# Kernel optimization log

Measured on AMD Instinct MI355X. Metric: run time of the kernel, lower is better.

The kernel has to match this reference:

```python
import jax, jax.numpy as jnp
import numpy as np

N, IN_F, OUT_F = 8192, 256, 128
ALPHA = 0.2          # LeakyReLU negative slope
NEG_INF = -9e15      # mask value used by the original module
DENSITY = 0.1        # adjacency density


def setup_inputs() -> dict:
    key = jax.random.key(0)
    k1, k2, k3, k4 = jax.random.split(key, 4)
    x = jax.random.normal(k1, (N, IN_F), dtype=jnp.float32)
    adj = (jax.random.uniform(k2, (N, N)) < DENSITY).astype(jnp.float32)
    W = jax.random.normal(k3, (IN_F, OUT_F), dtype=jnp.float32) * (1.0 / np.sqrt(IN_F))
    a = jax.random.normal(k4, (2 * OUT_F, 1), dtype=jnp.float32) * (1.0 / np.sqrt(2 * OUT_F))
    return {"x": x, "adj": adj, "W": W, "a": a}


def reference(x, adj, W, a):
    # h = x @ W : [N, F]
    h = x @ W
    # Decompose a^T [h_i ; h_j] = (h a1)_i + (h a2)_j  -- identical math to the
    # original O(N^2 * 2F) cat/repeat construction, without materializing it.
    a1 = a[:OUT_F, 0]           # [F]
    a2 = a[OUT_F:, 0]           # [F]
    s1 = h @ a1                 # [N]
    s2 = h @ a2                 # [N]
    e = jax.nn.leaky_relu(s1[:, None] + s2[None, :], negative_slope=ALPHA)  # [N, N]
    scores = jnp.where(adj > 0, e, NEG_INF)
    attention = jax.nn.softmax(scores, axis=1)   # row-wise softmax
    # dropout = 0.0 (eval mode) -> identity
    h_prime = attention @ h      # [N, F]
    return h_prime
```

## Files before the change

### kernel.cpp

```cpp
#include <hip/hip_runtime.h>
#include <hip/hip_bf16.h>

typedef __attribute__((ext_vector_type(4))) float  f32x4;
typedef __attribute__((ext_vector_type(8))) short  bf16x8;
typedef unsigned short u16;

#define ALPHA 0.2f
#define NN 8192
#define FF 128

extern "C" __global__ void __launch_bounds__(256)
gat_pre(const float* __restrict__ x, const float* __restrict__ Wm,
        const float* __restrict__ av, u16* __restrict__ hT,
        float* __restrict__ s1v, float* __restrict__ s2v) {
  __shared__ float xs[16][256];
  __shared__ float hs[16][128];
  const int t  = threadIdx.x;
  const int i0 = blockIdx.x * 16;

  {
    const int r = t >> 4, c0 = (t & 15) * 16;
    const f32x4* src = (const f32x4*)(x + (size_t)(i0 + r) * 256 + c0);
    f32x4* dst = (f32x4*)&xs[r][c0];
#pragma unroll
    for (int m = 0; m < 4; ++m) dst[m] = src[m];
  }
  __syncthreads();

  {
    const int c = t & 127, rh = t >> 7;
    float acc[8] = {0.f,0.f,0.f,0.f,0.f,0.f,0.f,0.f};
    for (int k = 0; k < 256; ++k) {
      const float wk = Wm[k * 128 + c];
#pragma unroll
      for (int r = 0; r < 8; ++r) acc[r] = fmaf(xs[rh * 8 + r][k], wk, acc[r]);
    }
#pragma unroll
    for (int r = 0; r < 8; ++r) hs[rh * 8 + r][c] = acc[r];
  }
  __syncthreads();

  {
    const int c = t >> 1, rr = (t & 1) * 8;
    u16 u[8];
#pragma unroll
    for (int k = 0; k < 8; ++k) {
      __hip_bfloat16 b = __float2bfloat16(hs[rr + k][c]);
      u[k] = *reinterpret_cast<u16*>(&b);
    }
    *(uint4*)(hT + (size_t)c * NN + i0 + rr) = *(const uint4*)u;
  }

  {
    const int r = t >> 4, q = t & 15;
    float p1 = 0.f, p2 = 0.f;
#pragma unroll
    for (int m = 0; m < 8; ++m) {
      const int c = q * 8 + m;
      const float hv = hs[r][c];
      p1 = fmaf(hv, av[c], p1);
      p2 = fmaf(hv, av[128 + c], p2);
    }
    p1 += __shfl_xor(p1, 1); p1 += __shfl_xor(p1, 2);
    p1 += __shfl_xor(p1, 4); p1 += __shfl_xor(p1, 8);
    p2 += __shfl_xor(p2, 1); p2 += __shfl_xor(p2, 2);
    p2 += __shfl_xor(p2, 4); p2 += __shfl_xor(p2, 8);
    if (q == 0) { s1v[i0 + r] = p1; s2v[i0 + r] = p2; }
  }
}

extern "C" __global__ void __launch_bounds__(512)
gat_main(const float* __restrict__ adj, const u16* __restrict__ hT,
         const float* __restrict__ s1v, const float* __restrict__ s2v,
         float* __restrict__ out) {
  __shared__ u16  wlds[32 * 128];
  __shared__ u16  hlds[128 * 128];
  __shared__ float denl[32];

  const int t    = threadIdx.x;
  const int lane = t & 63;
  const int i0   = blockIdx.x * 32;
  const int li   = t >> 4;
  const int j8   = (t & 15) * 8;
  const int wid  = t >> 6;
  const int rs   = wid & 1;
  const int cq   = wid >> 1;
  const int hc   = t >> 2;
  const int hq   = t & 3;

  const float s1i = s1v[i0 + li];
  const float* adjrow = adj + (size_t)(i0 + li) * NN + j8;
  const u16*   hrow   = hT + (size_t)hc * NN + hq * 32;

  f32x4 acc0 = {0.f,0.f,0.f,0.f}, acc1 = {0.f,0.f,0.f,0.f};
  float den = 0.f;

  f32x4 a0 = *(const f32x4*)(adjrow);
  f32x4 a1 = *(const f32x4*)(adjrow + 4);
  f32x4 z0 = *(const f32x4*)(s2v + j8);
  f32x4 z1 = *(const f32x4*)(s2v + j8 + 4);
  uint4 hr0 = *(const uint4*)(hrow);
  uint4 hr1 = *(const uint4*)(hrow + 8);
  uint4 hr2 = *(const uint4*)(hrow + 16);
  uint4 hr3 = *(const uint4*)(hrow + 24);

  for (int js = 0; js < NN; js += 128) {
    __syncthreads();

    {
      bf16x8 wpack;
      float dstep = 0.f;
#pragma unroll
      for (int e = 0; e < 8; ++e) {
        const float adv = (e < 4) ? a0[e] : a1[e - 4];
        const float tz  = s1i + ((e < 4) ? z0[e] : z1[e - 4]);
        const float fz  = tz > 0.f ? tz : ALPHA * tz;
        const float w8  = adv > 0.f ? __expf(fz) : 0.f;
        dstep += w8;
        __hip_bfloat16 hb = __float2bfloat16(w8);
        wpack[e] = *reinterpret_cast<short*>(&hb);
      }
      den += dstep;
      *(bf16x8*)((char*)wlds + ((li * 256 + j8 * 2) ^ ((li & 7) << 4))) = wpack;

      char* hb = (char*)hlds;
      const int base = hc * 256 + hq * 64;
      const int sw   = (hc & 7) << 4;
      *(uint4*)(hb + ((base +  0) ^ sw)) = hr0;
      *(uint4*)(hb + ((base + 16) ^ sw)) = hr1;
      *(uint4*)(hb + ((base + 32) ^ sw)) = hr2;
      *(uint4*)(hb + ((base + 48) ^ sw)) = hr3;
    }
    __syncthreads();

    if (js + 128 < NN) {
      const float* ap = adjrow + js + 128;
      a0 = *(const f32x4*)(ap);
      a1 = *(const f32x4*)(ap + 4);
      const float* zp = s2v + js + 128 + j8;
      z0 = *(const f32x4*)(zp);
      z1 = *(const f32x4*)(zp + 4);
      const u16* hp2 = hrow + js + 128;
      hr0 = *(const uint4*)(hp2);
      hr1 = *(const uint4*)(hp2 + 8);
      hr2 = *(const uint4*)(hp2 + 16);
      hr3 = *(const uint4*)(hp2 + 24);
    }

#pragma unroll
    for (int ks = 0; ks < 4; ++ks) {
      const int arow = rs * 16 + (lane & 15);
      const int koff = (ks * 32 + ((lane >> 4) << 3)) * 2;
      const bf16x8 af = *(const bf16x8*)((char*)wlds +
                          ((arow * 256 + koff) ^ ((arow & 7) << 4)));
      const int bc0 = cq * 32 + (lane & 15);
      const bf16x8 b0 = *(const bf16x8*)((char*)hlds +
                          ((bc0 * 256 + koff) ^ ((bc0 & 7) << 4)));
      const int bc1 = bc0 + 16;
      const bf16x8 b1 = *(const bf16x8*)((char*)hlds +
                          ((bc1 * 256 + koff) ^ ((bc1 & 7) << 4)));
      acc0 = __builtin_amdgcn_mfma_f32_16x16x32_bf16(af, b0, acc0, 0, 0, 0);
      acc1 = __builtin_amdgcn_mfma_f32_16x16x32_bf16(af, b1, acc1, 0, 0, 0);
    }
  }

  den += __shfl_xor(den, 1); den += __shfl_xor(den, 2);
  den += __shfl_xor(den, 4); den += __shfl_xor(den, 8);
  if ((t & 15) == 0) denl[li] = den;
  __syncthreads();

#pragma unroll
  for (int r = 0; r < 4; ++r) {
    const int row  = rs * 16 + ((lane >> 4) << 2) + r;
    const float dv = denl[row];
    const int col0 = cq * 32 + (lane & 15);
    out[(size_t)(i0 + row) * FF + col0]      = acc0[r] / dv;
    out[(size_t)(i0 + row) * FF + col0 + 16] = acc1[r] / dv;
  }
}

extern "C" void kernel_launch(void* const* d_in, const int* in_sizes, int n_in,
                              void* d_out, int out_size, void* d_ws, size_t ws_size,
                              hipStream_t stream) {
  const float* x   = (const float*)d_in[0];
  const float* adj = (const float*)d_in[1];
  const float* Wm  = (const float*)d_in[2];
  const float* av  = (const float*)d_in[3];
  float* out = (float*)d_out;

  u16*   hT  = (u16*)d_ws;
  float* s1v = (float*)((char*)d_ws + (size_t)FF * NN * 2);
  float* s2v = s1v + NN;

  gat_pre <<<NN / 16, 256, 0, stream>>>(x, Wm, av, hT, s1v, s2v);
  gat_main<<<NN / 32, 512, 0, stream>>>(adj, hT, s1v, s2v, out);
}
```

Measured before the change: 442.2 us.

## Split K across waves with direct global B-fragment loads and LDS reduction

Restructures the attention-aggregation kernel so that each of the 8 waves in a block handles a distinct slice of the neighbour (K) dimension for 16 rows. B fragments of hT are loaded straight from global memory into registers, which removes the per-iteration LDS staging and both __syncthreads. Partial accumulators and denominators are then reduced through LDS once at the end. The change also folds log2(e) into the precomputed scores so exp2 can be used, and replaces the adjacency branch with a multiply. The cost is more hT traffic through L2, since each block now rereads all of hT, and fewer rows per block.

```diff
diff --git a/kernel.cpp b/kernel.cpp
--- a/kernel.cpp
+++ b/kernel.cpp
@@ -8,6 +8,13 @@
 #define ALPHA 0.2f
 #define NN 8192
 #define FF 128
+#define LOG2E 1.4426950408889634f
+
+#if __has_builtin(__builtin_amdgcn_exp2f)
+#define EXP2F(x) __builtin_amdgcn_exp2f(x)
+#else
+#define EXP2F(x) __expf((x) * 0.6931471805599453f)
+#endif
 
 extern "C" __global__ void __launch_bounds__(256)
 gat_pre(const float* __restrict__ x, const float* __restrict__ Wm,
@@ -65,117 +72,97 @@
     p1 += __shfl_xor(p1, 4); p1 += __shfl_xor(p1, 8);
     p2 += __shfl_xor(p2, 1); p2 += __shfl_xor(p2, 2);
     p2 += __shfl_xor(p2, 4); p2 += __shfl_xor(p2, 8);
-    if (q == 0) { s1v[i0 + r] = p1; s2v[i0 + r] = p2; }
+    if (q == 0) { s1v[i0 + r] = p1 * LOG2E; s2v[i0 + r] = p2 * LOG2E; }
   }
 }
 
-extern "C" __global__ void __launch_bounds__(512)
+extern "C" __global__ void __launch_bounds__(512, 4)
 gat_main(const float* __restrict__ adj, const u16* __restrict__ hT,
-         const float* __restrict__ s1v, const float* __restrict__ s2v,
+         const float* __restrict__ s1l, const float* __restrict__ s2l,
          float* __restrict__ out) {
-  __shared__ u16  wlds[32 * 128];
-  __shared__ u16  hlds[128 * 128];
-  __shared__ float denl[32];
+  __shared__ float accp[8][16][132];
+  __shared__ float denp[8][16];
 
   const int t    = threadIdx.x;
   const int lane = t & 63;
-  const int i0   = blockIdx.x * 32;
-  const int li   = t >> 4;
-  const int j8   = (t & 15) * 8;
-  const int wid  = t >> 6;
-  const int rs   = wid & 1;
-  const int cq   = wid >> 1;
-  const int hc   = t >> 2;
-  const int hq   = t & 3;
+  const int wv   = t >> 6;
+  const int cA   = lane & 15;
+  const int kg   = lane >> 4;
+  const int i0   = blockIdx.x * 16;
+  const int jq0  = wv * (NN / 8);
 
-  const float s1i = s1v[i0 + li];
-  const float* adjrow = adj + (size_t)(i0 + li) * NN + j8;
-  const u16*   hrow   = hT + (size_t)hc * NN + hq * 32;
+  const float s1i = s1l[i0 + cA];
+  const float* adjp = adj + (size_t)(i0 + cA) * NN + jq0 + kg * 8;
+  const float* s2p  = s2l + jq0 + kg * 8;
+  const u16*   hTb  = hT + (size_t)cA * NN + jq0 + kg * 8;
 
-  f32x4 acc0 = {0.f,0.f,0.f,0.f}, acc1 = {0.f,0.f,0.f,0.f};
+  f32x4 acc[8];
+#pragma unroll
+  for (int f = 0; f < 8; ++f) acc[f] = (f32x4){0.f, 0.f, 0.f, 0.f};
   float den = 0.f;
 
-  f32x4 a0 = *(const f32x4*)(adjrow);
-  f32x4 a1 = *(const f32x4*)(adjrow + 4);
-  f32x4 z0 = *(const f32x4*)(s2v + j8);
-  f32x4 z1 = *(const f32x4*)(s2v + j8 + 4);
-  uint4 hr0 = *(const uint4*)(hrow);
-  uint4 hr1 = *(const uint4*)(hrow + 8);
-  uint4 hr2 = *(const uint4*)(hrow + 16);
-  uint4 hr3 = *(const uint4*)(hrow + 24);
+  f32x4 a0 = *(const f32x4*)(adjp);
+  f32x4 a1 = *(const f32x4*)(adjp + 4);
+  f32x4 z0 = *(const f32x4*)(s2p);
+  f32x4 z1 = *(const f32x4*)(s2p + 4);
 
-  for (int js = 0; js < NN; js += 128) {
-    __syncthreads();
+  for (int st = 0; st < 32; ++st) {
+    bf16x8 bf[8];
+#pragma unroll
+    for (int f = 0; f < 8; ++f)
+      bf[f] = *(const bf16x8*)(hTb + (size_t)f * 16 * NN + st * 32);
 
-    {
-      bf16x8 wpack;
-      float dstep = 0.f;
+    bf16x8 af;
+    float dstep = 0.f;
 #pragma unroll
-      for (int e = 0; e < 8; ++e) {
-        const float adv = (e < 4) ? a0[e] : a1[e - 4];
-        const float tz  = s1i + ((e < 4) ? z0[e] : z1[e - 4]);
-        const float fz  = tz > 0.f ? tz : ALPHA * tz;
-        const float w8  = adv > 0.f ? __expf(fz) : 0.f;
-        dstep += w8;
-        __hip_bfloat16 hb = __float2bfloat16(w8);
-        wpack[e] = *reinterpret_cast<short*>(&hb);
-      }
-      den += dstep;
-      *(bf16x8*)((char*)wlds + ((li * 256 + j8 * 2) ^ ((li & 7) << 4))) = wpack;
+    for (int e = 0; e < 8; ++e) {
+      const float adv = (e < 4) ? a0[e] : a1[e - 4];
+      const float tz  = s1i + ((e < 4) ? z0[e] : z1[e - 4]);
+      const float fz  = fmaxf(tz, ALPHA * tz);
+      const float w8  = adv * EXP2F(fz);
+      dstep += w8;
+      __hip_bfloat16 hb = __float2bfloat16(w8);
+      af[e] = *reinterpret_cast<short*>(&hb);
+    }
+    den += dstep;
 
-      char* hb = (char*)hlds;
-      const int base = hc * 256 + hq * 64;
-      const int sw   = (hc & 7) << 4;
-      *(uint4*)(hb + ((base +  0) ^ sw)) = hr0;
-      *(uint4*)(hb + ((base + 16) ^ sw)) = hr1;
-      *(uint4*)(hb + ((base + 32) ^ sw)) = hr2;
-      *(uint4*)(hb + ((base + 48) ^ sw)) = hr3;
-    }
-    __syncthreads();
-
-    if (js + 128 < NN) {
-      const float* ap = adjrow + js + 128;
+    if (st < 31) {
+      const float* ap = adjp + (st + 1) * 32;
       a0 = *(const f32x4*)(ap);
       a1 = *(const f32x4*)(ap + 4);
-      const float* zp = s2v + js + 128 + j8;
+      const float* zp = s2p + (st + 1) * 32;
       z0 = *(const f32x4*)(zp);
       z1 = *(const f32x4*)(zp + 4);
-      const u16* hp2 = hrow + js + 128;
-      hr0 = *(const uint4*)(hp2);
-      hr1 = *(const uint4*)(hp2 + 8);
-      hr2 = *(const uint4*)(hp2 + 16);
-      hr3 = *(const uint4*)(hp2 + 24);
     }
 
 #pragma unroll
-    for (int ks = 0; ks < 4; ++ks) {
-      const int arow = rs * 16 + (lane & 15);
-      const int koff = (ks * 32 + ((lane >> 4) << 3)) * 2;
-      const bf16x8 af = *(const bf16x8*)((char*)wlds +
-                          ((arow * 256 + koff) ^ ((arow & 7) << 4)));
-      const int bc0 = cq * 32 + (lane & 15);
-      const bf16x8 b0 = *(const bf16x8*)((char*)hlds +
-                          ((bc0 * 256 + koff) ^ ((bc0 & 7) << 4)));
-      const int bc1 = bc0 + 16;
-      const bf16x8 b1 = *(const bf16x8*)((char*)hlds +
-                          ((bc1 * 256 + koff) ^ ((bc1 & 7) << 4)));
-      acc0 = __builtin_amdgcn_mfma_f32_16x16x32_bf16(af, b0, acc0, 0, 0, 0);
-      acc1 = __builtin_amdgcn_mfma_f32_16x16x32_bf16(af, b1, acc1, 0, 0, 0);
-    }
+    for (int f = 0; f < 8; ++f)
+      acc[f] = __builtin_amdgcn_mfma_f32_16x16x32_bf16(af, bf[f], acc[f], 0, 0, 0);
   }
 
-  den += __shfl_xor(den, 1); den += __shfl_xor(den, 2);
-  den += __shfl_xor(den, 4); den += __shfl_xor(den, 8);
-  if ((t & 15) == 0) denl[li] = den;
+  den += __shfl_xor(den, 16);
+  den += __shfl_xor(den, 32);
+  if (kg == 0) denp[wv][cA] = den;
+
+#pragma unroll
+  for (int f = 0; f < 8; ++f)
+#pragma unroll
+    for (int r = 0; r < 4; ++r)
+      accp[wv][kg * 4 + r][f * 16 + cA] = acc[f][r];
+
   __syncthreads();
 
+  {
+    const int row = t >> 5;
+    const int c0  = (t & 31) * 4;
+    float dv = 0.f;
 #pragma unroll
-  for (int r = 0; r < 4; ++r) {
-    const int row  = rs * 16 + ((lane >> 4) << 2) + r;
-    const float dv = denl[row];
-    const int col0 = cq * 32 + (lane & 15);
-    out[(size_t)(i0 + row) * FF + col0]      = acc0[r] / dv;
-    out[(size_t)(i0 + row) * FF + col0 + 16] = acc1[r] / dv;
+    for (int w = 0; w < 8; ++w) dv += denp[w][row];
+    f32x4 s = {0.f, 0.f, 0.f, 0.f};
+#pragma unroll
+    for (int w = 0; w < 8; ++w) s += *(const f32x4*)&accp[w][row][c0];
+    s.x /= dv; s.y /= dv; s.z /= dv; s.w /= dv;
+    *(f32x4*)(out + (size_t)(i0 + row) * FF + c0) = s;
   }
 }
 
@@ -193,5 +180,5 @@
   float* s2v = s1v + NN;
 
   gat_pre <<<NN / 16, 256, 0, stream>>>(x, Wm, av, hT, s1v, s2v);
-  gat_main<<<NN / 32, 512, 0, stream>>>(adj, hT, s1v, s2v, out);
+  gat_main<<<NN / 16, 512, 0, stream>>>(adj, hT, s1v, s2v, out);
 }
```

New measurement: 512.3 us. +15.9%, slower.
